# Kernel tuning notes

Measured on AMD Instinct MI355X. Metric: run time of the kernel, lower is better.

## Reference

```python
import jax, jax.numpy as jnp
import numpy as np

SHAPES = ((96, 144), (48, 72), (24, 36), (12, 18))
BS, EMBED = 2, 256
HEADS, LEVELS, POINTS = 8, 4, 4
NEMBED = EMBED // HEADS
LEN_V = sum(h * w for h, w in SHAPES)
LEN_Q = LEN_V  # encoder self-attention: every pixel is a query


def _pos_grid_init():
    # Faithful re-implementation of MultiScaleDeformableAttention.pos_grid_init
    thetas = jnp.arange(HEADS, dtype=jnp.float32) * (2.0 * np.pi / HEADS)
    g = jnp.stack([jnp.cos(thetas), jnp.sin(thetas)], -1)
    g = g / jnp.max(jnp.abs(g), axis=-1, keepdims=True)
    g = jnp.tile(g.reshape(HEADS, 1, 1, 2), (1, LEVELS, POINTS, 1))
    scale = (jnp.arange(POINTS, dtype=jnp.float32) + 1.0)[None, None, :, None]
    return g * scale  # [HEADS, LEVELS, POINTS, 2]


def setup_inputs() -> dict:
    ks = jax.random.split(jax.random.key(0), 7)
    return {
        'query': jax.random.normal(ks[0], (BS, LEN_Q, EMBED), jnp.float32),
        'ref_points': jax.random.uniform(ks[1], (BS, LEN_Q, LEVELS, 2), jnp.float32),
        'value': jax.random.normal(ks[2], (BS, LEN_V, EMBED), jnp.float32),
        'pad_mask': jnp.ones((BS, LEN_V), dtype=bool),
        'value_proj_kernel': jax.random.normal(ks[3], (EMBED, HEADS, NEMBED), jnp.float32) * 0.05,
        'value_proj_bias': jnp.zeros((HEADS, NEMBED), jnp.float32),
        'sampling_offsets_kernel': jax.random.normal(ks[4], (EMBED, HEADS, LEVELS, POINTS, 2), jnp.float32) * 0.01,
        'sampling_offsets_bias': _pos_grid_init(),
        'attn_kernel': jax.random.normal(ks[5], (EMBED, HEADS, LEVELS * POINTS), jnp.float32) * 0.02,
        'attn_bias': jnp.zeros((HEADS, LEVELS * POINTS), jnp.float32),
        'out_kernel': jax.random.normal(ks[6], (HEADS, NEMBED, EMBED), jnp.float32) * 0.05,
        'out_bias': jnp.zeros((EMBED,), jnp.float32),
        'train': 0,
    }


def _bilinear(im, grid, w, h):
    """Batched 2D bilinear interpolation, zero outside the image.

    im:   [B, h*w, e] flattened feature map
    grid: [B, N, 2] normalized coords (pixel centers at (x+0.5)/w, (y+0.5)/h)
    Returns [B, N, e]. Identical math to the original gather-based kernel:
    out-of-bounds corner weights are zeroed, so zero-padding the image by 1
    reproduces the 'empty'-pad + masked-weight scheme exactly.
    """
    B, _, e = im.shape
    imp = jnp.pad(im.reshape(B, h, w, e), ((0, 0), (1, 1), (1, 1), (0, 0)))
    imp = imp.reshape(B, (h + 2) * (w + 2), e)
    x = grid[..., 0] * w - 0.5
    y = grid[..., 1] * h - 0.5
    x0 = jnp.floor(x).astype(jnp.int32)
    y0 = jnp.floor(y).astype(jnp.int32)
    x1 = x0 + 1
    y1 = y0 + 1

    def gather(yy, xx):
        idx = jnp.clip(yy + 1, 0, h + 1) * (w + 2) + jnp.clip(xx + 1, 0, w + 1)
        return jnp.take_along_axis(imp, idx[..., None], axis=1)  # [B, N, e]

    x0f, y0f = x0.astype(x.dtype), y0.astype(y.dtype)
    x1f, y1f = x1.astype(x.dtype), y1.astype(y.dtype)
    inx0 = (x0 >= 0) & (x0 <= w - 1)
    inx1 = (x1 >= 0) & (x1 <= w - 1)
    iny0 = (y0 >= 0) & (y0 <= h - 1)
    iny1 = (y1 >= 0) & (y1 <= h - 1)
    wa = jnp.where(inx0 & iny0, (x1f - x) * (y1f - y), 0.0)
    wb = jnp.where(inx0 & iny1, (x1f - x) * (y - y0f), 0.0)
    wc = jnp.where(inx1 & iny0, (x - x0f) * (y1f - y), 0.0)
    wd = jnp.where(inx1 & iny1, (x - x0f) * (y - y0f), 0.0)
    return (gather(y0, x0) * wa[..., None] + gather(y1, x0) * wb[..., None]
            + gather(y0, x1) * wc[..., None] + gather(y1, x1) * wd[..., None])


def _forward(query, ref_points, value, pad_mask, vpk, vpb, sok, sob, ak, ab, okern, obias):
    bs, len_q, _ = query.shape
    len_v = value.shape[1]
    # value projection + pad masking -> [bs*H, len_v, nembed]
    v = jnp.einsum('bve,ehd->bvhd', value, vpk) + vpb
    v = jnp.where(pad_mask[..., None, None], v, 0)
    v = v.transpose(0, 2, 1, 3).reshape(bs * HEADS, len_v, NEMBED)
    # sampling locations (ref_dim == 2 branch) -> [bs*H, L, P*len_q, 2]
    off = jnp.einsum('bqe,ehlpc->bqhlpc', query, sok) + sob
    offset_norm = jnp.array([[w, h] for h, w in SHAPES], dtype=query.dtype)  # [L, 2]
    loc = ref_points[:, :, None, :, None, :] + off / offset_norm[None, None, None, :, None, :]
    loc = loc.transpose(0, 2, 3, 4, 1, 5).reshape(bs * HEADS, LEVELS, POINTS * len_q, 2)
    # attention weights (softmax over L*P) -> [bs*H, len_q, L*P]
    aw = jnp.einsum('bqe,ehm->bqhm', query, ak) + ab
    aw = jax.nn.softmax(aw, axis=-1)
    aw = aw.transpose(0, 2, 1, 3).reshape(bs * HEADS, len_q, LEVELS * POINTS)
    # per-level bilinear sampling, concatenated level-major over (level, point)
    starts = np.cumsum([0] + [h * w for h, w in SHAPES])
    sampled = []
    for li, (h, w) in enumerate(SHAPES):
        vl = v[:, starts[li]:starts[li + 1], :]
        s = _bilinear(vl, loc[:, li], w, h)  # [bs*H, P*len_q, nembed]
        sampled.append(s.reshape(bs * HEADS, POINTS, len_q, NEMBED))
    sampled = jnp.concatenate(sampled, axis=1)  # [bs*H, L*P, len_q, nembed]
    x = jnp.einsum('blqe,bql->bqe', sampled, aw)
    x = x.reshape(bs, HEADS, len_q, NEMBED)
    # output projection: DenseGeneral over (heads, nembed)
    return jnp.einsum('bhqe,hed->bqd', x, okern) + obias


def reference(query, ref_points, value, pad_mask, value_proj_kernel, value_proj_bias,
              sampling_offsets_kernel, sampling_offsets_bias, attn_kernel, attn_bias,
              out_kernel, out_bias, train):
    del train  # eval mode (no remat); math is identical
    return _forward(query, ref_points, value, pad_mask, value_proj_kernel, value_proj_bias,
                    sampling_offsets_kernel, sampling_offsets_bias, attn_kernel, attn_bias,
                    out_kernel, out_bias)
```

## Files before the change

kernel.cpp:

```cpp
#include <hip/hip_runtime.h>
#include <math.h>

#define LEN 18360
#define M_ROWS (2 * LEN)
#define NTASK (16 * LEN)

typedef unsigned short u16;
typedef __attribute__((ext_vector_type(8))) short bf16x8;
typedef __attribute__((ext_vector_type(4))) float f32x4;

__device__ __forceinline__ u16 f2bf(float f) {
  unsigned u = __float_as_uint(f);
  return (u16)((u + 0x7fffu + ((u >> 16) & 1u)) >> 16);
}
__device__ __forceinline__ void async_cp16(const void* g, void* l) {
  __builtin_amdgcn_global_load_lds(
      (const __attribute__((address_space(1))) unsigned*)g,
      (__attribute__((address_space(3))) unsigned*)l, 16, 0, 0);
}

__global__ __launch_bounds__(256) void gemm_mfma_k(
    const u16* __restrict__ A0, const u16* __restrict__ Bt0,
    const float* __restrict__ bias0, void* __restrict__ C0, int N0, int nt0,
    int mode0, int split, const u16* __restrict__ A1,
    const u16* __restrict__ Bt1, const float* __restrict__ bias1,
    void* __restrict__ C1, int N1, int nt1, int mode1) {
  __shared__ u16 A_lds[8 * 512];
  __shared__ u16 B_lds[8 * 512];

  int bid = (int)blockIdx.x;
  const u16* A;
  const u16* Bt;
  const float* bias;
  void* Cv;
  int N, nt, mode;
  if (bid < split) {
    A = A0; Bt = Bt0; bias = bias0; Cv = C0; N = N0; nt = nt0; mode = mode0;
  } else {
    bid -= split;
    A = A1; Bt = Bt1; bias = bias1; Cv = C1; N = N1; nt = nt1; mode = mode1;
  }
  const int n0 = (bid % nt) << 7;
  const int m0 = (bid / nt) << 7;

  const int tid = threadIdx.x;
  const int w = tid >> 6;
  const int lane = tid & 63;
  const int wm = w & 1, wn = w >> 1;
  const int mr = lane & 15;
  const int kq = (lane >> 4) * 8;

  f32x4 acc[4][4];
#pragma unroll
  for (int i = 0; i < 4; i++)
#pragma unroll
    for (int j = 0; j < 4; j++) acc[i][j] = (f32x4){0.f, 0.f, 0.f, 0.f};

  for (int k0 = 0; k0 < 256; k0 += 32) {
    __syncthreads();
#pragma unroll
    for (int t = 0; t < 2; t++) {
      const int st = 2 * w + t;
      const int ga = min(m0 + st * 16 + mr, M_ROWS - 1);
      async_cp16(A + (size_t)ga * 256 + k0 + kq, &A_lds[st * 512]);
      const int gb = n0 + st * 16 + mr;
      async_cp16(Bt + (size_t)gb * 256 + k0 + kq, &B_lds[st * 512]);
    }
    __syncthreads();

    bf16x8 af[4], bf[4];
#pragma unroll
    for (int i = 0; i < 4; i++)
      af[i] = *(const bf16x8*)&A_lds[(wm * 4 + i) * 512 + lane * 8];
#pragma unroll
    for (int j = 0; j < 4; j++)
      bf[j] = *(const bf16x8*)&B_lds[(wn * 4 + j) * 512 + lane * 8];
#pragma unroll
    for (int i = 0; i < 4; i++)
#pragma unroll
      for (int j = 0; j < 4; j++)
        acc[i][j] = __builtin_amdgcn_mfma_f32_16x16x32_bf16(bf[j], af[i],
                                                            acc[i][j], 0, 0, 0);
  }

#pragma unroll
  for (int i = 0; i < 4; i++) {
    const int row = m0 + wm * 64 + i * 16 + mr;
    if (row >= M_ROWS) continue;
#pragma unroll
    for (int j = 0; j < 4; j++) {
      const int col = n0 + wn * 64 + j * 16 + (lane >> 4) * 4;
      const float4 b4 = *(const float4*)(bias + col);
      float4 o;
      o.x = acc[i][j][0] + b4.x;
      o.y = acc[i][j][1] + b4.y;
      o.z = acc[i][j][2] + b4.z;
      o.w = acc[i][j][3] + b4.w;
      if (mode == 0) {
        *(float4*)((float*)Cv + (size_t)row * N + col) = o;
      } else if (mode == 1) {
        const int b = row >= LEN;
        const int lv = row - b * LEN;
        const int h = col >> 5, d = col & 31;
        uint2 p;
        p.x = (unsigned)f2bf(o.x) | ((unsigned)f2bf(o.y) << 16);
        p.y = (unsigned)f2bf(o.z) | ((unsigned)f2bf(o.w) << 16);
        *(uint2*)((u16*)Cv + ((size_t)((b * 8 + h) * LEN + lv)) * 32 + d) = p;
      } else {
        uint2 p;
        p.x = (unsigned)f2bf(o.x) | ((unsigned)f2bf(o.y) << 16);
        p.y = (unsigned)f2bf(o.z) | ((unsigned)f2bf(o.w) << 16);
        *(uint2*)((u16*)Cv + (size_t)row * N + col) = p;
      }
    }
  }
}

__global__ __launch_bounds__(256) void cast_qv_k(const float* __restrict__ q,
                                                 const float* __restrict__ v,
                                                 u16* __restrict__ qb,
                                                 u16* __restrict__ vb) {
  const size_t i = ((size_t)blockIdx.x * 256 + threadIdx.x) * 4;
  float4 a = *(const float4*)(q + i);
  uint2 p;
  p.x = (unsigned)f2bf(a.x) | ((unsigned)f2bf(a.y) << 16);
  p.y = (unsigned)f2bf(a.z) | ((unsigned)f2bf(a.w) << 16);
  *(uint2*)&qb[i] = p;
  float4 c = *(const float4*)(v + i);
  p.x = (unsigned)f2bf(c.x) | ((unsigned)f2bf(c.y) << 16);
  p.y = (unsigned)f2bf(c.z) | ((unsigned)f2bf(c.w) << 16);
  *(uint2*)&vb[i] = p;
}

__global__ __launch_bounds__(256) void wcast_k(
    const float* __restrict__ vpk, const float* __restrict__ sok,
    const float* __restrict__ ak, const float* __restrict__ ok,
    const float* __restrict__ sob, const float* __restrict__ ab,
    u16* __restrict__ vpk_t, u16* __restrict__ sa_t, u16* __restrict__ ok_t,
    float* __restrict__ bias_cat) {
  const int gid = blockIdx.x * 256 + threadIdx.x;
  if (gid < 65536) {
    const int d = gid, n = d >> 8, k = d & 255;
    vpk_t[d] = f2bf(vpk[k * 256 + n]);
  } else if (gid < 131072) {
    const int d = gid - 65536, n = d >> 8, k = d & 255;
    sa_t[d] = f2bf(sok[k * 256 + n]);
  } else if (gid < 163840) {
    const int d = gid - 131072, n = d >> 8, k = d & 255;
    sa_t[65536 + d] = f2bf(ak[k * 128 + n]);
  } else if (gid < 229376) {
    const int d = gid - 163840, n = d >> 8, k = d & 255;
    ok_t[d] = f2bf(ok[k * 256 + n]);
  } else if (gid < 229760) {
    const int d = gid - 229376;
    bias_cat[d] = (d < 256) ? sob[d] : ab[d - 256];
  }
}

__global__ __launch_bounds__(256) void sampler_k(
    const u16* __restrict__ v,
    const u16* __restrict__ offaw,
    const float* __restrict__ refp,
    u16* __restrict__ xb)
{
  __shared__ int2 meta[4][258];
  const int tid = threadIdx.x;

  const int cW[4] = {144, 72, 36, 18};
  const int cH[4] = {96, 48, 24, 12};
  const int cS[4] = {0, 13824, 17280, 18144};

  {
    const int t = tid >> 4;
    const int s = tid & 15;
    const int l = s >> 2;

    const int task = (blockIdx.x << 4) + t;
    const int q = task % LEN;
    const int bh = task / LEN;
    const int h = bh & 7;
    const int b = bh >> 3;
    const size_t qrow = (size_t)(b * LEN + q);
    const u16* rowp = offaw + qrow * 384;

    const float logit = __uint_as_float((unsigned)rowp[256 + h * 16 + s] << 16);
    float mx = logit;
#pragma unroll
    for (int m = 1; m < 16; m <<= 1) mx = fmaxf(mx, __shfl_xor(mx, m, 16));
    const float e = __expf(logit - mx);
    float ssum = e;
#pragma unroll
    for (int m = 1; m < 16; m <<= 1) ssum += __shfl_xor(ssum, m, 16);
    const float wsm = e / ssum;

    const int W = cW[l], H = cH[l], ST = cS[l];
    const float2 rp = ((const float2*)(refp + qrow * 8))[l];
    const unsigned upair = ((const unsigned*)(rowp + h * 32))[s];
    const float ox = __uint_as_float(upair << 16);
    const float oy = __uint_as_float(upair & 0xffff0000u);
    const float X = rp.x * (float)W + ox - 0.5f;
    const float Y = rp.y * (float)H + oy - 0.5f;
    const float fx = floorf(X), fy = floorf(Y);
    const int x0 = (int)fx, y0 = (int)fy;
    const float dx = X - fx, dy = Y - fy;
    const float ux = 1.f - dx, uy = 1.f - dy;
    const bool bx0 = (unsigned)x0 < (unsigned)W;
    const bool bx1 = (unsigned)(x0 + 1) < (unsigned)W;
    const bool by0 = (unsigned)y0 < (unsigned)H;
    const bool by1 = (unsigned)(y0 + 1) < (unsigned)H;
    const int xc0 = min(max(x0, 0), W - 1);
    const int xc1 = min(max(x0 + 1, 0), W - 1);
    const int yc0 = min(max(y0, 0), H - 1);
    const int yc1 = min(max(y0 + 1, 0), H - 1);
    const float w00 = (bx0 & by0) ? wsm * ux * uy : 0.f;
    const float w10 = (bx1 & by0) ? wsm * dx * uy : 0.f;
    const float w01 = (bx0 & by1) ? wsm * ux * dy : 0.f;
    const float w11 = (bx1 & by1) ? wsm * dx * dy : 0.f;

    meta[0][tid] = make_int2((ST + yc0 * W + xc0) << 6, __float_as_int(w00));
    meta[1][tid] = make_int2((ST + yc0 * W + xc1) << 6, __float_as_int(w10));
    meta[2][tid] = make_int2((ST + yc1 * W + xc0) << 6, __float_as_int(w01));
    meta[3][tid] = make_int2((ST + yc1 * W + xc1) << 6, __float_as_int(w11));
  }
  __syncthreads();

  const int u = tid >> 5;
  const int lane = tid & 31;
  const int c = lane >> 3;
  const int dq = lane & 7;

#pragma unroll
  for (int rep = 0; rep < 2; rep++) {
    const int t = u + rep * 8;
    const int task = (blockIdx.x << 4) + t;
    const int q = task % LEN;
    const int bh = task / LEN;
    const int h = bh & 7;
    const int b = bh >> 3;
    const size_t qrow = (size_t)(b * LEN + q);
    const char* vb = (const char*)v + (size_t)bh * LEN * 64;

    float4 acc = make_float4(0.f, 0.f, 0.f, 0.f);
#pragma unroll
    for (int s = 0; s < 16; s++) {
      const int2 m2 = meta[c][t * 16 + s];
      const float wgt = __int_as_float(m2.y);
      const uint2 pv = *(const uint2*)(vb + (size_t)(unsigned)m2.x + (dq << 3));
      acc.x = fmaf(wgt, __uint_as_float(pv.x << 16), acc.x);
      acc.y = fmaf(wgt, __uint_as_float(pv.x & 0xffff0000u), acc.y);
      acc.z = fmaf(wgt, __uint_as_float(pv.y << 16), acc.z);
      acc.w = fmaf(wgt, __uint_as_float(pv.y & 0xffff0000u), acc.w);
    }
#pragma unroll
    for (int m = 8; m <= 16; m <<= 1) {
      acc.x += __shfl_xor(acc.x, m, 32);
      acc.y += __shfl_xor(acc.y, m, 32);
      acc.z += __shfl_xor(acc.z, m, 32);
      acc.w += __shfl_xor(acc.w, m, 32);
    }
    if (c == 0) {
      uint2 p;
      p.x = (unsigned)f2bf(acc.x) | ((unsigned)f2bf(acc.y) << 16);
      p.y = (unsigned)f2bf(acc.z) | ((unsigned)f2bf(acc.w) << 16);
      *(uint2*)&xb[qrow * 256 + h * 32 + (dq << 2)] = p;
    }
  }
}

extern "C" void kernel_launch(void* const* d_in, const int* in_sizes, int n_in,
                              void* d_out, int out_size, void* d_ws,
                              size_t ws_size, hipStream_t stream) {
  (void)in_sizes; (void)n_in; (void)out_size; (void)ws_size;

  const float* query = (const float*)d_in[0];
  const float* refp = (const float*)d_in[1];
  const float* value = (const float*)d_in[2];
  const float* vpk = (const float*)d_in[4];
  const float* vpb = (const float*)d_in[5];
  const float* sok = (const float*)d_in[6];
  const float* sob = (const float*)d_in[7];
  const float* ak = (const float*)d_in[8];
  const float* ab = (const float*)d_in[9];
  const float* okern = (const float*)d_in[10];
  const float* obias = (const float*)d_in[11];

  char* p = (char*)d_ws;
  u16* v_ws = (u16*)p;   p += (size_t)M_ROWS * 256 * 2;
  u16* offaw = (u16*)p;  p += (size_t)M_ROWS * 384 * 2;
  u16* qbf = (u16*)p;    p += (size_t)M_ROWS * 256 * 2;
  u16* vbf = (u16*)p;    p += (size_t)M_ROWS * 256 * 2;
  u16* vpk_t = (u16*)p;  p += 65536 * 2;
  u16* sa_t = (u16*)p;   p += 98304 * 2;
  u16* ok_t = (u16*)p;   p += 65536 * 2;
  float* bias_cat = (float*)p;
  u16* x_b = qbf;

  const dim3 blk(256);
  const int mt = (M_ROWS + 127) / 128;

  cast_qv_k<<<dim3(2350080 / 256), blk, 0, stream>>>(query, value, qbf, vbf);
  wcast_k<<<dim3(898), blk, 0, stream>>>(vpk, sok, ak, okern, sob, ab, vpk_t,
                                         sa_t, ok_t, bias_cat);
  gemm_mfma_k<<<dim3(2 * mt + 3 * mt), blk, 0, stream>>>(
      vbf, vpk_t, vpb, v_ws, 256, 2, 1, 2 * mt,
      qbf, sa_t, bias_cat, offaw, 384, 3, 2);
  sampler_k<<<dim3(NTASK / 16), blk, 0, stream>>>(v_ws, offaw, refp, x_b);
  gemm_mfma_k<<<dim3(2 * mt), blk, 0, stream>>>(
      x_b, ok_t, obias, (float*)d_out, 256, 2, 0, 2 * mt,
      x_b, ok_t, obias, (float*)d_out, 256, 2, 0);
}
```

Baseline: 275.5 us.

## Merge prep kernels, drop LDS in GEMM, store values as fp16, widen sampler loads

Several unrelated changes ship together. The two cast kernels become one launch, and the weight transpose now goes through a shared-memory tile so reads are coalesced. The GEMM stops staging operands through LDS and loads each MFMA fragment straight from global memory, which removes the barriers but relies on cache for operand reuse. The value projection is written as fp16 instead of bf16, and the sampler reads 16 bytes per lane with a new meta layout and fewer shuffle steps. Storing values as fp16 adds overflow and precision risk if projected values are large.

```diff
diff --git a/kernel.cpp b/kernel.cpp
--- a/kernel.cpp
+++ b/kernel.cpp
@@ -1,4 +1,5 @@
 #include <hip/hip_runtime.h>
+#include <hip/hip_fp16.h>
 #include <math.h>
 
 #define LEN 18360
@@ -12,11 +13,6 @@
 __device__ __forceinline__ u16 f2bf(float f) {
   unsigned u = __float_as_uint(f);
   return (u16)((u + 0x7fffu + ((u >> 16) & 1u)) >> 16);
-}
-__device__ __forceinline__ void async_cp16(const void* g, void* l) {
-  __builtin_amdgcn_global_load_lds(
-      (const __attribute__((address_space(1))) unsigned*)g,
-      (__attribute__((address_space(3))) unsigned*)l, 16, 0, 0);
 }
 
 __global__ __launch_bounds__(256) void gemm_mfma_k(
@@ -25,9 +21,6 @@
     int mode0, int split, const u16* __restrict__ A1,
     const u16* __restrict__ Bt1, const float* __restrict__ bias1,
     void* __restrict__ C1, int N1, int nt1, int mode1) {
-  __shared__ u16 A_lds[8 * 512];
-  __shared__ u16 B_lds[8 * 512];
-
   int bid = (int)blockIdx.x;
   const u16* A;
   const u16* Bt;
@@ -50,31 +43,29 @@
   const int mr = lane & 15;
   const int kq = (lane >> 4) * 8;
 
+  const u16* arow[4];
+  const u16* brow[4];
+#pragma unroll
+  for (int i = 0; i < 4; i++) {
+    const int ga = min(m0 + wm * 64 + i * 16 + mr, M_ROWS - 1);
+    arow[i] = A + (size_t)ga * 256 + kq;
+    const int gb = n0 + wn * 64 + i * 16 + mr;
+    brow[i] = Bt + (size_t)gb * 256 + kq;
+  }
+
   f32x4 acc[4][4];
 #pragma unroll
   for (int i = 0; i < 4; i++)
 #pragma unroll
     for (int j = 0; j < 4; j++) acc[i][j] = (f32x4){0.f, 0.f, 0.f, 0.f};
 
+#pragma unroll 2
   for (int k0 = 0; k0 < 256; k0 += 32) {
-    __syncthreads();
-#pragma unroll
-    for (int t = 0; t < 2; t++) {
-      const int st = 2 * w + t;
-      const int ga = min(m0 + st * 16 + mr, M_ROWS - 1);
-      async_cp16(A + (size_t)ga * 256 + k0 + kq, &A_lds[st * 512]);
-      const int gb = n0 + st * 16 + mr;
-      async_cp16(Bt + (size_t)gb * 256 + k0 + kq, &B_lds[st * 512]);
-    }
-    __syncthreads();
-
     bf16x8 af[4], bf[4];
 #pragma unroll
-    for (int i = 0; i < 4; i++)
-      af[i] = *(const bf16x8*)&A_lds[(wm * 4 + i) * 512 + lane * 8];
-#pragma unroll
-    for (int j = 0; j < 4; j++)
-      bf[j] = *(const bf16x8*)&B_lds[(wn * 4 + j) * 512 + lane * 8];
+    for (int i = 0; i < 4; i++) af[i] = *(const bf16x8*)(arow[i] + k0);
+#pragma unroll
+    for (int j = 0; j < 4; j++) bf[j] = *(const bf16x8*)(brow[j] + k0);
 #pragma unroll
     for (int i = 0; i < 4; i++)
 #pragma unroll
@@ -102,9 +93,11 @@
         const int b = row >= LEN;
         const int lv = row - b * LEN;
         const int h = col >> 5, d = col & 31;
+        __half2 ha = __floats2half2_rn(o.x, o.y);
+        __half2 hb = __floats2half2_rn(o.z, o.w);
         uint2 p;
-        p.x = (unsigned)f2bf(o.x) | ((unsigned)f2bf(o.y) << 16);
-        p.y = (unsigned)f2bf(o.z) | ((unsigned)f2bf(o.w) << 16);
+        p.x = *(unsigned*)&ha;
+        p.y = *(unsigned*)&hb;
         *(uint2*)((u16*)Cv + ((size_t)((b * 8 + h) * LEN + lv)) * 32 + d) = p;
       } else {
         uint2 p;
@@ -116,45 +109,52 @@
   }
 }
 
-__global__ __launch_bounds__(256) void cast_qv_k(const float* __restrict__ q,
-                                                 const float* __restrict__ v,
-                                                 u16* __restrict__ qb,
-                                                 u16* __restrict__ vb) {
-  const size_t i = ((size_t)blockIdx.x * 256 + threadIdx.x) * 4;
-  float4 a = *(const float4*)(q + i);
-  uint2 p;
-  p.x = (unsigned)f2bf(a.x) | ((unsigned)f2bf(a.y) << 16);
-  p.y = (unsigned)f2bf(a.z) | ((unsigned)f2bf(a.w) << 16);
-  *(uint2*)&qb[i] = p;
-  float4 c = *(const float4*)(v + i);
-  p.x = (unsigned)f2bf(c.x) | ((unsigned)f2bf(c.y) << 16);
-  p.y = (unsigned)f2bf(c.z) | ((unsigned)f2bf(c.w) << 16);
-  *(uint2*)&vb[i] = p;
-}
-
-__global__ __launch_bounds__(256) void wcast_k(
-    const float* __restrict__ vpk, const float* __restrict__ sok,
-    const float* __restrict__ ak, const float* __restrict__ ok,
-    const float* __restrict__ sob, const float* __restrict__ ab,
-    u16* __restrict__ vpk_t, u16* __restrict__ sa_t, u16* __restrict__ ok_t,
+__global__ __launch_bounds__(256) void prep_k(
+    const float* __restrict__ q, const float* __restrict__ v,
+    u16* __restrict__ qb, u16* __restrict__ vb, const float* __restrict__ vpk,
+    const float* __restrict__ sok, const float* __restrict__ ak,
+    const float* __restrict__ ok, const float* __restrict__ sob,
+    const float* __restrict__ ab, u16* __restrict__ vpk_t,
+    u16* __restrict__ sa_t, u16* __restrict__ ok_t,
     float* __restrict__ bias_cat) {
-  const int gid = blockIdx.x * 256 + threadIdx.x;
-  if (gid < 65536) {
-    const int d = gid, n = d >> 8, k = d & 255;
-    vpk_t[d] = f2bf(vpk[k * 256 + n]);
-  } else if (gid < 131072) {
-    const int d = gid - 65536, n = d >> 8, k = d & 255;
-    sa_t[d] = f2bf(sok[k * 256 + n]);
-  } else if (gid < 163840) {
-    const int d = gid - 131072, n = d >> 8, k = d & 255;
-    sa_t[65536 + d] = f2bf(ak[k * 128 + n]);
-  } else if (gid < 229376) {
-    const int d = gid - 163840, n = d >> 8, k = d & 255;
-    ok_t[d] = f2bf(ok[k * 256 + n]);
-  } else if (gid < 229760) {
-    const int d = gid - 229376;
-    bias_cat[d] = (d < 256) ? sob[d] : ab[d - 256];
-  }
+  __shared__ float tile[32][33];
+  const int bid = blockIdx.x, tid = threadIdx.x;
+  if (bid < 9180) {
+    const size_t i = ((size_t)bid * 256 + tid) * 4;
+    float4 a = *(const float4*)(q + i);
+    uint2 p;
+    p.x = (unsigned)f2bf(a.x) | ((unsigned)f2bf(a.y) << 16);
+    p.y = (unsigned)f2bf(a.z) | ((unsigned)f2bf(a.w) << 16);
+    *(uint2*)&qb[i] = p;
+    float4 c = *(const float4*)(v + i);
+    p.x = (unsigned)f2bf(c.x) | ((unsigned)f2bf(c.y) << 16);
+    p.y = (unsigned)f2bf(c.z) | ((unsigned)f2bf(c.w) << 16);
+    *(uint2*)&vb[i] = p;
+    return;
+  }
+  int tb = bid - 9180;
+  if (tb < 224) {
+    const float* src;
+    u16* dst;
+    int ncols, lt;
+    if (tb < 64) { src = vpk; dst = vpk_t; ncols = 256; lt = tb; }
+    else if (tb < 128) { src = sok; dst = sa_t; ncols = 256; lt = tb - 64; }
+    else if (tb < 160) { src = ak; dst = sa_t + 65536; ncols = 128; lt = tb - 128; }
+    else { src = ok; dst = ok_t; ncols = 256; lt = tb - 160; }
+    const int ntx = ncols >> 5;
+    const int k0 = (lt / ntx) << 5, c0 = (lt % ntx) << 5;
+    const int r = tid >> 5, cc = tid & 31;
+#pragma unroll
+    for (int p = 0; p < 4; p++)
+      tile[r + 8 * p][cc] = src[(size_t)(k0 + r + 8 * p) * ncols + c0 + cc];
+    __syncthreads();
+#pragma unroll
+    for (int p = 0; p < 4; p++)
+      dst[(size_t)(c0 + r + 8 * p) * 256 + k0 + cc] = f2bf(tile[cc][r + 8 * p]);
+    return;
+  }
+  for (int i = tid; i < 384; i += 256)
+    bias_cat[i] = (i < 256) ? sob[i] : ab[i - 256];
 }
 
 __global__ __launch_bounds__(256) void sampler_k(
@@ -163,7 +163,7 @@
     const float* __restrict__ refp,
     u16* __restrict__ xb)
 {
-  __shared__ int2 meta[4][258];
+  __shared__ int2 meta[16 * 66];
   const int tid = threadIdx.x;
 
   const int cW[4] = {144, 72, 36, 18};
@@ -171,11 +171,11 @@
   const int cS[4] = {0, 13824, 17280, 18144};
 
   {
-    const int t = tid >> 4;
+    const int T = tid >> 4;
     const int s = tid & 15;
     const int l = s >> 2;
 
-    const int task = (blockIdx.x << 4) + t;
+    const int task = (blockIdx.x << 4) + T;
     const int q = task % LEN;
     const int bh = task / LEN;
     const int h = bh & 7;
@@ -217,53 +217,58 @@
     const float w01 = (bx0 & by1) ? wsm * ux * dy : 0.f;
     const float w11 = (bx1 & by1) ? wsm * dx * dy : 0.f;
 
-    meta[0][tid] = make_int2((ST + yc0 * W + xc0) << 6, __float_as_int(w00));
-    meta[1][tid] = make_int2((ST + yc0 * W + xc1) << 6, __float_as_int(w10));
-    meta[2][tid] = make_int2((ST + yc1 * W + xc0) << 6, __float_as_int(w01));
-    meta[3][tid] = make_int2((ST + yc1 * W + xc1) << 6, __float_as_int(w11));
+    int2* mp = &meta[T * 66 + s * 4];
+    mp[0] = make_int2((ST + yc0 * W + xc0) << 6, __float_as_int(w00));
+    mp[1] = make_int2((ST + yc0 * W + xc1) << 6, __float_as_int(w10));
+    mp[2] = make_int2((ST + yc1 * W + xc0) << 6, __float_as_int(w01));
+    mp[3] = make_int2((ST + yc1 * W + xc1) << 6, __float_as_int(w11));
   }
   __syncthreads();
 
-  const int u = tid >> 5;
-  const int lane = tid & 31;
-  const int c = lane >> 3;
-  const int dq = lane & 7;
-
-#pragma unroll
-  for (int rep = 0; rep < 2; rep++) {
-    const int t = u + rep * 8;
-    const int task = (blockIdx.x << 4) + t;
-    const int q = task % LEN;
-    const int bh = task / LEN;
-    const int h = bh & 7;
-    const int b = bh >> 3;
-    const size_t qrow = (size_t)(b * LEN + q);
-    const char* vb = (const char*)v + (size_t)bh * LEN * 64;
-
-    float4 acc = make_float4(0.f, 0.f, 0.f, 0.f);
-#pragma unroll
-    for (int s = 0; s < 16; s++) {
-      const int2 m2 = meta[c][t * 16 + s];
-      const float wgt = __int_as_float(m2.y);
-      const uint2 pv = *(const uint2*)(vb + (size_t)(unsigned)m2.x + (dq << 3));
-      acc.x = fmaf(wgt, __uint_as_float(pv.x << 16), acc.x);
-      acc.y = fmaf(wgt, __uint_as_float(pv.x & 0xffff0000u), acc.y);
-      acc.z = fmaf(wgt, __uint_as_float(pv.y << 16), acc.z);
-      acc.w = fmaf(wgt, __uint_as_float(pv.y & 0xffff0000u), acc.w);
+  const int wv = tid >> 6;
+  const int lane = tid & 63;
+  const int T = wv * 4 + (lane >> 4);
+  const int c = (lane >> 2) & 3;
+  const int dq = lane & 3;
+
+  const int task = (blockIdx.x << 4) + T;
+  const int q = task % LEN;
+  const int bh = task / LEN;
+  const int h = bh & 7;
+  const int b = bh >> 3;
+  const size_t qrow = (size_t)(b * LEN + q);
+  const char* vb = (const char*)v + (size_t)bh * LEN * 64;
+
+  float acc[8];
+#pragma unroll
+  for (int j = 0; j < 8; j++) acc[j] = 0.f;
+
+#pragma unroll
+  for (int s = 0; s < 16; s++) {
+    const int2 m2 = meta[T * 66 + s * 4 + c];
+    const float wgt = __int_as_float(m2.y);
+    const uint4 pv =
+        *(const uint4*)(vb + (size_t)(unsigned)m2.x + (dq << 4));
+    const __half2* h2 = (const __half2*)&pv;
+#pragma unroll
+    for (int j = 0; j < 4; j++) {
+      const float2 f = __half22float2(h2[j]);
+      acc[2 * j] = fmaf(wgt, f.x, acc[2 * j]);
+      acc[2 * j + 1] = fmaf(wgt, f.y, acc[2 * j + 1]);
     }
-#pragma unroll
-    for (int m = 8; m <= 16; m <<= 1) {
-      acc.x += __shfl_xor(acc.x, m, 32);
-      acc.y += __shfl_xor(acc.y, m, 32);
-      acc.z += __shfl_xor(acc.z, m, 32);
-      acc.w += __shfl_xor(acc.w, m, 32);
-    }
-    if (c == 0) {
-      uint2 p;
-      p.x = (unsigned)f2bf(acc.x) | ((unsigned)f2bf(acc.y) << 16);
-      p.y = (unsigned)f2bf(acc.z) | ((unsigned)f2bf(acc.w) << 16);
-      *(uint2*)&xb[qrow * 256 + h * 32 + (dq << 2)] = p;
-    }
+  }
+#pragma unroll
+  for (int m = 4; m <= 8; m <<= 1)
+#pragma unroll
+    for (int j = 0; j < 8; j++) acc[j] += __shfl_xor(acc[j], m, 64);
+
+  if (c == 0) {
+    uint4 p;
+    p.x = (unsigned)f2bf(acc[0]) | ((unsigned)f2bf(acc[1]) << 16);
+    p.y = (unsigned)f2bf(acc[2]) | ((unsigned)f2bf(acc[3]) << 16);
+    p.z = (unsigned)f2bf(acc[4]) | ((unsigned)f2bf(acc[5]) << 16);
+    p.w = (unsigned)f2bf(acc[6]) | ((unsigned)f2bf(acc[7]) << 16);
+    *(uint4*)&xb[qrow * 256 + h * 32 + (dq << 3)] = p;
   }
 }
 
@@ -298,9 +303,9 @@
   const dim3 blk(256);
   const int mt = (M_ROWS + 127) / 128;
 
-  cast_qv_k<<<dim3(2350080 / 256), blk, 0, stream>>>(query, value, qbf, vbf);
-  wcast_k<<<dim3(898), blk, 0, stream>>>(vpk, sok, ak, okern, sob, ab, vpk_t,
-                                         sa_t, ok_t, bias_cat);
+  prep_k<<<dim3(9405), blk, 0, stream>>>(query, value, qbf, vbf, vpk, sok, ak,
+                                         okern, sob, ab, vpk_t, sa_t, ok_t,
+                                         bias_cat);
   gemm_mfma_k<<<dim3(2 * mt + 3 * mt), blk, 0, stream>>>(
       vbf, vpk_t, vpb, v_ws, 256, 2, 1, 2 * mt,
       qbf, sa_t, bias_cat, offaw, 384, 3, 2);
```

Measured after the change: 276.1 us. Within noise of the previous version (+0.2%).
